# Kernel optimization log

Hardware: AMD Instinct MI355X
Metric: run time of the kernel (lower is better)

The kernel has to match this reference:

```python
import jax, jax.numpy as jnp
import numpy as np

B, L, D, V, T = 4, 512, 2048, 32000, 1024


def setup_inputs() -> dict:
    key = jax.random.key(0)
    k1, k2, k3 = jax.random.split(key, 3)
    encoder_outs = jax.random.normal(k1, (B, L, D), dtype=jnp.float32)
    embed_weight = jax.random.normal(k2, (V, D), dtype=jnp.float32) * 0.02
    input_ids = jax.random.randint(k3, (B, T), 0, V)
    # encoder (audio) tokens occupy the prefix of the LLM input sequence
    modality_mask = jnp.broadcast_to(jnp.arange(T) < L, (B, T))
    return {
        "encoder_outs": encoder_outs,
        "embed_weight": embed_weight,
        "input_ids": input_ids,
        "modality_mask": modality_mask,
    }


def reference(encoder_outs, embed_weight, input_ids, modality_mask):
    # chunked matmul in torch == one big contraction: (B,L,D) x (V,D) -> (B,L,V)
    sim = jnp.einsum("bld,vd->blv", encoder_outs, embed_weight)
    enc_norm = jnp.sqrt(jnp.sum(jnp.square(encoder_outs), axis=-1, keepdims=True))
    w_norm = jnp.sqrt(jnp.sum(jnp.square(embed_weight), axis=-1))  # (V,)
    cosine = sim / enc_norm / w_norm[None, None, :]
    quantize_index = jnp.argmax(cosine, axis=-1)  # (B, L)
    enc_quant = embed_weight[quantize_index]      # (B, L, D) gather lookup

    inputs_embeds = embed_weight[input_ids]       # (B, T, D)
    # pad encoder tokens to full sequence length, then blend via modality mask
    enc_pad = jnp.pad(enc_quant, ((0, 0), (0, T - L), (0, 0)))
    blended = jnp.where(modality_mask[:, :, None], enc_pad, inputs_embeds)
    return blended, quantize_index
```

## Files before the change

kernel.cpp:

```cpp
#include <hip/hip_runtime.h>
#include <hip/hip_fp8.h>
#include <math.h>

typedef __attribute__((ext_vector_type(8))) short short8v;
typedef __attribute__((ext_vector_type(4))) float f32x4;
typedef unsigned long long u64;
typedef unsigned short ushort_t;
typedef unsigned char u8;

constexpr int Bb = 4;
constexpr int Ll = 512;
constexpr int Dk = 2048;
constexpr int Vv = 32000;
constexpr int Tt = 1024;
constexpr int Mrows = Bb * Ll;

constexpr int BM = 256;
constexpr int BN = 256;
constexpr int BK = 64;
constexpr int NKT = Dk / BK;
constexpr int NBX = Mrows / BM;
constexpr int NBY = Vv / BN;
constexpr int NWG = NBX * NBY;
constexpr int CHUNK = NWG / 8;
constexpr int TILE_BYTES = 32 * 512;

constexpr int KCAND = 8;
constexpr int CAND_STRIDE = 500;

constexpr int FBM = 128;
constexpr int FBN = 128;
constexpr int FNVB = Vv / FBN;

constexpr size_t WS_NEEDED = 16842752ull + 65536000ull;

__device__ __forceinline__ unsigned int fkey(float f) {
    unsigned int u = __float_as_uint(f);
    return (u & 0x80000000u) ? ~u : (u | 0x80000000u);
}
__device__ __forceinline__ void top2(u64& b1, u64& b2, u64 p) {
    if (p > b1) { b2 = b1; b1 = p; }
    else if (p > b2) { b2 = p; }
}
__device__ __forceinline__ u64 shfl64(u64 x, int m) {
    unsigned lo = __shfl_xor((unsigned)x, m, 64);
    unsigned hi = __shfl_xor((unsigned)(x >> 32), m, 64);
    return ((u64)hi << 32) | lo;
}
__device__ __forceinline__ u8 to_e4m3(float x) {
    __hip_fp8_e4m3 q(x);
    return q.__x;
}
__device__ __forceinline__ void gload_lds16(const void* g, void* l) {
    __builtin_amdgcn_global_load_lds(
        (const __attribute__((address_space(1))) unsigned int*)g,
        (__attribute__((address_space(3))) unsigned int*)l, 16, 0, 0);
}

__global__ __launch_bounds__(256) void convertA_fp8(const float* __restrict__ A,
                                                    u8* __restrict__ At) {
    const int row = blockIdx.x * 4 + (threadIdx.x >> 6);
    const int lane = threadIdx.x & 63;
    const int bx = row >> 8, rg = (row & 255) >> 4, r15 = row & 15;
    const float* src = A + (size_t)row * Dk;
#pragma unroll
    for (int i = 0; i < 4; ++i) {
        const int k0 = (i * 64 + lane) * 8;
        float4 x = *(const float4*)(src + k0);
        float4 y = *(const float4*)(src + k0 + 4);
        u8 o[8] = {to_e4m3(x.x), to_e4m3(x.y), to_e4m3(x.z), to_e4m3(x.w),
                   to_e4m3(y.x), to_e4m3(y.y), to_e4m3(y.z), to_e4m3(y.w)};
        const int t = k0 >> 6, c = (k0 >> 5) & 1, lp = r15 + ((k0 >> 3) & 3) * 16;
        *(u64*)(At + ((size_t)(bx * NKT + t) * 32 + rg * 2 + c) * 512 + lp * 8) =
            *(const u64*)o;
    }
}

__global__ __launch_bounds__(256) void convertW_fp8(const float* __restrict__ W,
                                                    u8* __restrict__ Wt,
                                                    float* __restrict__ winv) {
    const int row = blockIdx.x * 4 + (threadIdx.x >> 6);
    const int lane = threadIdx.x & 63;
    const int by = row >> 8, rg = (row & 255) >> 4, r15 = row & 15;
    const float* src = W + (size_t)row * Dk;
    float sq = 0.f;
#pragma unroll
    for (int i = 0; i < 4; ++i) {
        const int k0 = (i * 64 + lane) * 8;
        float4 x = *(const float4*)(src + k0);
        float4 y = *(const float4*)(src + k0 + 4);
        sq = fmaf(x.x, x.x, sq); sq = fmaf(x.y, x.y, sq);
        sq = fmaf(x.z, x.z, sq); sq = fmaf(x.w, x.w, sq);
        sq = fmaf(y.x, y.x, sq); sq = fmaf(y.y, y.y, sq);
        sq = fmaf(y.z, y.z, sq); sq = fmaf(y.w, y.w, sq);
        u8 o[8] = {to_e4m3(x.x * 64.f), to_e4m3(x.y * 64.f), to_e4m3(x.z * 64.f),
                   to_e4m3(x.w * 64.f), to_e4m3(y.x * 64.f), to_e4m3(y.y * 64.f),
                   to_e4m3(y.z * 64.f), to_e4m3(y.w * 64.f)};
        const int t = k0 >> 6, c = (k0 >> 5) & 1, lp = r15 + ((k0 >> 3) & 3) * 16;
        *(u64*)(Wt + ((size_t)(by * NKT + t) * 32 + rg * 2 + c) * 512 + lp * 8) =
            *(const u64*)o;
    }
#pragma unroll
    for (int off = 32; off; off >>= 1) sq += __shfl_down(sq, off, 64);
    if (lane == 0) winv[row] = 1.0f / sqrtf(sq);
}

__global__ __launch_bounds__(256) void wnorm_kernel(const float* __restrict__ W,
                                                    float* __restrict__ winv) {
    int wave = (blockIdx.x * blockDim.x + threadIdx.x) >> 6;
    int lane = threadIdx.x & 63;
    if (wave >= Vv) return;
    const float4* row = (const float4*)(W + (size_t)wave * Dk);
    float s = 0.f;
#pragma unroll
    for (int i = 0; i < Dk / 4 / 64; ++i) {
        float4 v = row[lane + 64 * i];
        s = fmaf(v.x, v.x, s); s = fmaf(v.y, v.y, s);
        s = fmaf(v.z, v.z, s); s = fmaf(v.w, v.w, s);
    }
#pragma unroll
    for (int off = 32; off; off >>= 1) s += __shfl_down(s, off, 64);
    if (lane == 0) winv[wave] = 1.0f / sqrtf(s);
}

__global__ void init_best_kernel(u64* __restrict__ best) {
    int i = blockIdx.x * blockDim.x + threadIdx.x;
    if (i < Mrows) best[i] = 0ull;
}

__global__ __launch_bounds__(1024, 4) void score_topk_kernel(
    const u8* __restrict__ At, const u8* __restrict__ Wt,
    const float* __restrict__ winv, u64* __restrict__ cand) {
    __shared__ __align__(16) u8 Alds[2][TILE_BYTES];
    __shared__ __align__(16) u8 Wlds[2][TILE_BYTES];

    const int orig = blockIdx.x;
    const int swz = (orig & 7) * CHUNK + (orig >> 3);
    const int bx = swz & (NBX - 1);
    const int by = swz >> 3;
    const int row0 = bx * BM;
    const int v0 = by * BN;

    const int tid = threadIdx.x;
    const int lane = tid & 63;
    const int w = tid >> 6;
    const int wrr = w >> 2;
    const int wcc = w & 3;

    const u8* sA = At + (size_t)bx * NKT * TILE_BYTES + w * 1024 + lane * 16;
    const u8* sW = Wt + (size_t)by * NKT * TILE_BYTES + w * 1024 + lane * 16;

    f32x4 acc[4][4];
#pragma unroll
    for (int i = 0; i < 4; ++i)
#pragma unroll
        for (int j = 0; j < 4; ++j) acc[i][j] = (f32x4){0.f, 0.f, 0.f, 0.f};

    gload_lds16(sA, &Alds[0][w * 1024]);
    gload_lds16(sW, &Wlds[0][w * 1024]);
    __syncthreads();

    int cur = 0;
    for (int t = 0; t < NKT; ++t) {
        if (t + 1 < NKT) {
            const size_t off = (size_t)(t + 1) * TILE_BYTES;
            gload_lds16(sA + off, &Alds[cur ^ 1][w * 1024]);
            gload_lds16(sW + off, &Wlds[cur ^ 1][w * 1024]);
        }
        __builtin_amdgcn_s_setprio(1);
#pragma unroll
        for (int c = 0; c < 2; ++c) {
            long long a[4], b[4];
#pragma unroll
            for (int m = 0; m < 4; ++m)
                a[m] = *(const long long*)&Alds[cur][(((wrr * 4 + m) * 2 + c) * 64 + lane) * 8];
#pragma unroll
            for (int n = 0; n < 4; ++n)
                b[n] = *(const long long*)&Wlds[cur][(((wcc * 4 + n) * 2 + c) * 64 + lane) * 8];
#pragma unroll
            for (int m = 0; m < 4; ++m)
#pragma unroll
                for (int n = 0; n < 4; ++n)
                    acc[m][n] = __builtin_amdgcn_mfma_f32_16x16x32_fp8_fp8(
                        a[m], b[n], acc[m][n], 0, 0, 0);
        }
        __builtin_amdgcn_s_setprio(0);
        __syncthreads();
        cur ^= 1;
    }

    const int cb = lane & 15;
    float wv[4];
#pragma unroll
    for (int n = 0; n < 4; ++n) wv[n] = winv[v0 + wcc * 64 + n * 16 + cb];

    u64(*red)[8] = (u64(*)[8]) & Alds[0][0];
#pragma unroll
    for (int m = 0; m < 4; ++m) {
#pragma unroll
        for (int reg = 0; reg < 4; ++reg) {
            u64 b1 = 0, b2 = 0;
#pragma unroll
            for (int n = 0; n < 4; ++n) {
                float s = acc[m][n][reg] * wv[n];
                int v = v0 + wcc * 64 + n * 16 + cb;
                u64 p = ((u64)fkey(s) << 32) | (unsigned)(Vv - 1 - v);
                top2(b1, b2, p);
            }
#pragma unroll
            for (int msk = 1; msk < 16; msk <<= 1) {
                u64 o1 = shfl64(b1, msk);
                u64 o2 = shfl64(b2, msk);
                top2(b1, b2, o1);
                top2(b1, b2, o2);
            }
            if (cb == 0) {
                int rl = wrr * 64 + m * 16 + ((lane >> 4) << 2) + reg;
                red[rl][wcc * 2] = b1;
                red[rl][wcc * 2 + 1] = b2;
            }
        }
    }
    __syncthreads();
    if (tid < BM) {
        u64 b1 = red[tid][0], b2 = red[tid][1];
#pragma unroll
        for (int j = 2; j < 8; ++j) top2(b1, b2, red[tid][j]);
        u64* c = cand + (size_t)(row0 + tid) * CAND_STRIDE + by * 2;
        c[0] = b1;
        c[1] = b2;
    }
}

template <typename LdsT>
__device__ __forceinline__ void topk_epilogue_f(f32x4 (&acc)[4][4], LdsT* ldsbase,
                                                const float* __restrict__ winv,
                                                u64* __restrict__ cand, int row0, int v0,
                                                int vby, int tid, int lane, int wr,
                                                int wc) {
    const int cbase = v0 + wc * 64 + (lane & 15);
    float wv[4];
#pragma unroll
    for (int nf = 0; nf < 4; ++nf) wv[nf] = winv[cbase + nf * 16];

    u64(*red)[4] = (u64(*)[4])ldsbase;
#pragma unroll
    for (int mf = 0; mf < 4; ++mf) {
#pragma unroll
        for (int reg = 0; reg < 4; ++reg) {
            u64 b1 = 0, b2 = 0;
#pragma unroll
            for (int nf = 0; nf < 4; ++nf) {
                float s = acc[mf][nf][reg] * wv[nf];
                int v = cbase + nf * 16;
                u64 p = ((u64)fkey(s) << 32) | (unsigned)(Vv - 1 - v);
                top2(b1, b2, p);
            }
#pragma unroll
            for (int m = 1; m < 16; m <<= 1) {
                u64 o1 = shfl64(b1, m);
                u64 o2 = shfl64(b2, m);
                top2(b1, b2, o1);
                top2(b1, b2, o2);
            }
            if ((lane & 15) == 0) {
                int rl = wr * 64 + mf * 16 + ((lane >> 4) << 2) + reg;
                red[rl][wc * 2] = b1;
                red[rl][wc * 2 + 1] = b2;
            }
        }
    }
    __syncthreads();
    if (tid < FBM) {
        u64 b1 = red[tid][0], b2 = red[tid][1];
        top2(b1, b2, red[tid][2]);
        top2(b1, b2, red[tid][3]);
        u64* c = cand + (size_t)(row0 + tid) * CAND_STRIDE + vby * 2;
        c[0] = b1;
        c[1] = b2;
    }
}

__global__ __launch_bounds__(256) void score_topk_fallback(
    const float* __restrict__ A, const float* __restrict__ W,
    const float* __restrict__ winv, u64* __restrict__ cand) {
    __shared__ __align__(16) short Albuf[4096];
    __shared__ __align__(16) short Wlbuf[4096];

    const int tid = threadIdx.x;
    const int row0 = blockIdx.x * FBM;
    const int v0 = blockIdx.y * FBN;
    const int lane = tid & 63;
    const int wid = tid >> 6;
    const int wr = wid >> 1, wc = wid & 1;

    const int rA = ((tid >> 6) << 4) + (tid & 15);
    const int kk = ((tid >> 4) & 3) * 8;

    const float* pa = A + (size_t)(row0 + rA) * Dk + kk;
    const float* pw = W + (size_t)(v0 + rA) * Dk + kk;

    float4 fa0, fa1, fa2, fa3, fw0, fw1, fw2, fw3;
    auto ld4 = [](const float* p) { return *(const float4*)p; };
    auto load_regs = [&](int k0) {
        fa0 = ld4(pa + k0); fa1 = ld4(pa + k0 + 4);
        fa2 = ld4(pa + k0 + (size_t)64 * Dk); fa3 = ld4(pa + k0 + (size_t)64 * Dk + 4);
        fw0 = ld4(pw + k0); fw1 = ld4(pw + k0 + 4);
        fw2 = ld4(pw + k0 + (size_t)64 * Dk); fw3 = ld4(pw + k0 + (size_t)64 * Dk + 4);
    };
    auto pk = [](float lo, float hi) {
        return (int)((__float_as_uint(lo) >> 16) | (__float_as_uint(hi) & 0xFFFF0000u));
    };
    auto cv = [&](float4 a, float4 b) {
        int4 r; r.x = pk(a.x, a.y); r.y = pk(a.z, a.w);
        r.z = pk(b.x, b.y); r.w = pk(b.z, b.w); return r;
    };
    auto write_lds = [&]() {
        *(int4*)(Albuf + tid * 8) = cv(fa0, fa1);
        *(int4*)(Albuf + tid * 8 + 2048) = cv(fa2, fa3);
        *(int4*)(Wlbuf + tid * 8) = cv(fw0, fw1);
        *(int4*)(Wlbuf + tid * 8 + 2048) = cv(fw2, fw3);
    };

    f32x4 acc[4][4];
#pragma unroll
    for (int i = 0; i < 4; ++i)
#pragma unroll
        for (int j = 0; j < 4; ++j) acc[i][j] = (f32x4){0.f, 0.f, 0.f, 0.f};

    load_regs(0);
    for (int kt = 0; kt < Dk / 32; ++kt) {
        write_lds();
        __syncthreads();
        if (kt + 1 < Dk / 32) load_regs((kt + 1) * 32);
        short8v af[4], bf[4];
        const short8v* Ap = (const short8v*)Albuf;
        const short8v* Wp = (const short8v*)Wlbuf;
#pragma unroll
        for (int mf = 0; mf < 4; ++mf) af[mf] = Ap[(wr * 4 + mf) * 64 + lane];
#pragma unroll
        for (int nf = 0; nf < 4; ++nf) bf[nf] = Wp[(wc * 4 + nf) * 64 + lane];
#pragma unroll
        for (int mf = 0; mf < 4; ++mf)
#pragma unroll
            for (int nf = 0; nf < 4; ++nf)
                acc[mf][nf] = __builtin_amdgcn_mfma_f32_16x16x32_bf16(
                    af[mf], bf[nf], acc[mf][nf], 0, 0, 0);
        __syncthreads();
    }

    topk_epilogue_f(acc, Albuf, winv, cand, row0, v0, blockIdx.y, tid, lane, wr, wc);
}

__global__ __launch_bounds__(256) void topk_kernel(const u64* __restrict__ cand,
                                                   int* __restrict__ sel, int nents) {
    int row = blockIdx.x * 4 + (threadIdx.x >> 6);
    int lane = threadIdx.x & 63;
    if (row >= Mrows) return;
    const u64* c = cand + (size_t)row * CAND_STRIDE;
    u64 v[8];
#pragma unroll
    for (int i = 0; i < 8; ++i) {
        int idx = lane + i * 64;
        v[i] = (idx < nents) ? c[idx] : 0ull;
    }
#pragma unroll
    for (int it = 0; it < KCAND; ++it) {
        u64 lm = 0;
#pragma unroll
        for (int i = 0; i < 8; ++i) lm = v[i] > lm ? v[i] : lm;
#pragma unroll
        for (int m = 32; m; m >>= 1) {
            u64 o = shfl64(lm, m);
            lm = o > lm ? o : lm;
        }
#pragma unroll
        for (int i = 0; i < 8; ++i)
            if (v[i] == lm) v[i] = 0;
        if (lane == 0) sel[row * KCAND + it] = Vv - 1 - (int)(unsigned)(lm & 0xFFFFFFFFu);
    }
}

__global__ __launch_bounds__(256) void rescore_kernel(
    const float* __restrict__ A, const float* __restrict__ W,
    const float* __restrict__ winv, const int* __restrict__ sel,
    u64* __restrict__ best) {
    int gw = (int)((blockIdx.x * blockDim.x + threadIdx.x) >> 6);
    int lane = threadIdx.x & 63;
    if (gw >= Mrows * KCAND) return;
    int row = gw >> 3, c = gw & 7;
    int v = sel[row * KCAND + c];
    const float4* a = (const float4*)(A + (size_t)row * Dk);
    const float4* w = (const float4*)(W + (size_t)v * Dk);
    float s = 0.f;
#pragma unroll
    for (int i = 0; i < Dk / 4 / 64; ++i) {
        float4 x = a[lane + 64 * i], y = w[lane + 64 * i];
        s = fmaf(x.x, y.x, s); s = fmaf(x.y, y.y, s);
        s = fmaf(x.z, y.z, s); s = fmaf(x.w, y.w, s);
    }
#pragma unroll
    for (int m = 32; m; m >>= 1) s += __shfl_xor(s, m, 64);
    if (lane == 0) {
        u64 p = ((u64)fkey(s * winv[v]) << 32) | (unsigned)(Vv - 1 - v);
        atomicMax(best + row, p);
    }
}

__global__ __launch_bounds__(256) void blend_kernel(
    const float* __restrict__ emb, const int* __restrict__ ids,
    const u64* __restrict__ best, float* __restrict__ out) {
    int row = blockIdx.x;
    int b = row / Tt;
    int t = row % Tt;
    int idx;
    if (t < Ll) {
        idx = Vv - 1 - (int)(best[b * Ll + t] & 0xFFFFFFFFu);
    } else {
        idx = ids[row];
    }
    const float4* src = (const float4*)(emb + (size_t)idx * Dk);
    float4* dst = (float4*)(out + (size_t)row * Dk);
    for (int i = threadIdx.x; i < Dk / 4; i += blockDim.x) dst[i] = src[i];
    if (t < Ll && threadIdx.x == 0) {
        out[(size_t)Bb * Tt * Dk + (size_t)(b * Ll + t)] = (float)idx;
    }
}

extern "C" void kernel_launch(void* const* d_in, const int* in_sizes, int n_in,
                              void* d_out, int out_size, void* d_ws, size_t ws_size,
                              hipStream_t stream) {
    const float* encoder_outs = (const float*)d_in[0];
    const float* embed_weight = (const float*)d_in[1];
    const int* input_ids = (const int*)d_in[2];

    float* out = (float*)d_out;

    float* winv = (float*)d_ws;
    u64* best = (u64*)((char*)d_ws + 131072);
    int* sel = (int*)((char*)d_ws + 147456);
    u64* cand = (u64*)((char*)d_ws + 262144);
    u8* At = (u8*)((char*)d_ws + 8454144);
    u8* Wt = (u8*)((char*)d_ws + 16842752);

    init_best_kernel<<<(Mrows + 255) / 256, 256, 0, stream>>>(best);

    if (ws_size >= WS_NEEDED) {
        convertA_fp8<<<Mrows / 4, 256, 0, stream>>>(encoder_outs, At);
        convertW_fp8<<<Vv / 4, 256, 0, stream>>>(embed_weight, Wt, winv);
        score_topk_kernel<<<NWG, 1024, 0, stream>>>(At, Wt, winv, cand);
        topk_kernel<<<Mrows / 4, 256, 0, stream>>>(cand, sel, 2 * NBY);
    } else {
        wnorm_kernel<<<Vv * 64 / 256, 256, 0, stream>>>(embed_weight, winv);
        dim3 grid(Mrows / FBM, Vv / FBN);
        score_topk_fallback<<<grid, 256, 0, stream>>>(encoder_outs, embed_weight, winv,
                                                      cand);
        topk_kernel<<<Mrows / 4, 256, 0, stream>>>(cand, sel, 2 * FNVB);
    }
    rescore_kernel<<<Mrows * KCAND / 4, 256, 0, stream>>>(encoder_outs, embed_weight,
                                                          winv, sel, best);
    blend_kernel<<<Bb * Tt, 256, 0, stream>>>(embed_weight, input_ids, best, out);
}
```

Measured before the change: 947.6 us.

## Load FP8 GEMM fragments directly from global into registers, dropping LDS staging

The fp8 scoring GEMM no longer stages A and W tiles through double-buffered LDS with global_load_lds and per-step barriers. Each wave now loads 16-byte fragments straight from global memory into registers, with two register buffers in flight. The conversion kernels rewrite the packed layout so that one 16-byte load covers both k-halves. The workgroup shrinks to 512 threads, each wave computing 8x4 MFMA tiles. This removes LDS traffic and __syncthreads, but operands shared across waves are now re-read from global/L2 instead of reused from LDS, and register pressure rises.

Result: slower. 1.346 ms (+42.0%).

```diff
diff --git a/kernel.cpp b/kernel.cpp
--- a/kernel.cpp
+++ b/kernel.cpp
@@ -4,6 +4,7 @@
 
 typedef __attribute__((ext_vector_type(8))) short short8v;
 typedef __attribute__((ext_vector_type(4))) float f32x4;
+typedef __attribute__((ext_vector_type(2))) long long i64x2;
 typedef unsigned long long u64;
 typedef unsigned short ushort_t;
 typedef unsigned char u8;
@@ -17,13 +18,12 @@
 
 constexpr int BM = 256;
 constexpr int BN = 256;
-constexpr int BK = 64;
-constexpr int NKT = Dk / BK;
+constexpr int NKT = 32;
 constexpr int NBX = Mrows / BM;
 constexpr int NBY = Vv / BN;
 constexpr int NWG = NBX * NBY;
 constexpr int CHUNK = NWG / 8;
-constexpr int TILE_BYTES = 32 * 512;
+constexpr int TSTRIDE = 16 * 1024;
 
 constexpr int KCAND = 8;
 constexpr int CAND_STRIDE = 500;
@@ -50,11 +50,6 @@
 __device__ __forceinline__ u8 to_e4m3(float x) {
     __hip_fp8_e4m3 q(x);
     return q.__x;
-}
-__device__ __forceinline__ void gload_lds16(const void* g, void* l) {
-    __builtin_amdgcn_global_load_lds(
-        (const __attribute__((address_space(1))) unsigned int*)g,
-        (__attribute__((address_space(3))) unsigned int*)l, 16, 0, 0);
 }
 
 __global__ __launch_bounds__(256) void convertA_fp8(const float* __restrict__ A,
@@ -71,7 +66,7 @@
         u8 o[8] = {to_e4m3(x.x), to_e4m3(x.y), to_e4m3(x.z), to_e4m3(x.w),
                    to_e4m3(y.x), to_e4m3(y.y), to_e4m3(y.z), to_e4m3(y.w)};
         const int t = k0 >> 6, c = (k0 >> 5) & 1, lp = r15 + ((k0 >> 3) & 3) * 16;
-        *(u64*)(At + ((size_t)(bx * NKT + t) * 32 + rg * 2 + c) * 512 + lp * 8) =
+        *(u64*)(At + ((size_t)(bx * NKT + t) * 16 + rg) * 1024 + lp * 16 + c * 8) =
             *(const u64*)o;
     }
 }
@@ -97,7 +92,7 @@
                    to_e4m3(x.w * 64.f), to_e4m3(y.x * 64.f), to_e4m3(y.y * 64.f),
                    to_e4m3(y.z * 64.f), to_e4m3(y.w * 64.f)};
         const int t = k0 >> 6, c = (k0 >> 5) & 1, lp = r15 + ((k0 >> 3) & 3) * 16;
-        *(u64*)(Wt + ((size_t)(by * NKT + t) * 32 + rg * 2 + c) * 512 + lp * 8) =
+        *(u64*)(Wt + ((size_t)(by * NKT + t) * 16 + rg) * 1024 + lp * 16 + c * 8) =
             *(const u64*)o;
     }
 #pragma unroll
@@ -128,11 +123,10 @@
     if (i < Mrows) best[i] = 0ull;
 }
 
-__global__ __launch_bounds__(1024, 4) void score_topk_kernel(
+__global__ __launch_bounds__(512, 2) void score_topk_kernel(
     const u8* __restrict__ At, const u8* __restrict__ Wt,
     const float* __restrict__ winv, u64* __restrict__ cand) {
-    __shared__ __align__(16) u8 Alds[2][TILE_BYTES];
-    __shared__ __align__(16) u8 Wlds[2][TILE_BYTES];
+    __shared__ __align__(16) u64 red[256][8];
 
     const int orig = blockIdx.x;
     const int swz = (orig & 7) * CHUNK + (orig >> 3);
@@ -144,66 +138,61 @@
     const int tid = threadIdx.x;
     const int lane = tid & 63;
     const int w = tid >> 6;
-    const int wrr = w >> 2;
-    const int wcc = w & 3;
-
-    const u8* sA = At + (size_t)bx * NKT * TILE_BYTES + w * 1024 + lane * 16;
-    const u8* sW = Wt + (size_t)by * NKT * TILE_BYTES + w * 1024 + lane * 16;
-
-    f32x4 acc[4][4];
-#pragma unroll
-    for (int i = 0; i < 4; ++i)
+    const int wr = w >> 2;
+    const int wc = w & 3;
+
+    const u8* pA = At + (size_t)bx * NKT * TSTRIDE + (wr * 8) * 1024 + lane * 16;
+    const u8* pW = Wt + (size_t)by * NKT * TSTRIDE + (wc * 4) * 1024 + lane * 16;
+
+    f32x4 acc[8][4];
+#pragma unroll
+    for (int i = 0; i < 8; ++i)
 #pragma unroll
         for (int j = 0; j < 4; ++j) acc[i][j] = (f32x4){0.f, 0.f, 0.f, 0.f};
 
-    gload_lds16(sA, &Alds[0][w * 1024]);
-    gload_lds16(sW, &Wlds[0][w * 1024]);
-    __syncthreads();
-
-    int cur = 0;
-    for (int t = 0; t < NKT; ++t) {
-        if (t + 1 < NKT) {
-            const size_t off = (size_t)(t + 1) * TILE_BYTES;
-            gload_lds16(sA + off, &Alds[cur ^ 1][w * 1024]);
-            gload_lds16(sW + off, &Wlds[cur ^ 1][w * 1024]);
-        }
-        __builtin_amdgcn_s_setprio(1);
-#pragma unroll
-        for (int c = 0; c < 2; ++c) {
-            long long a[4], b[4];
-#pragma unroll
-            for (int m = 0; m < 4; ++m)
-                a[m] = *(const long long*)&Alds[cur][(((wrr * 4 + m) * 2 + c) * 64 + lane) * 8];
-#pragma unroll
-            for (int n = 0; n < 4; ++n)
-                b[n] = *(const long long*)&Wlds[cur][(((wcc * 4 + n) * 2 + c) * 64 + lane) * 8];
-#pragma unroll
-            for (int m = 0; m < 4; ++m)
+    i64x2 fa0[8], fw0[4], fa1[8], fw1[4];
+    auto LD = [&](int t, i64x2 (&fa)[8], i64x2 (&fw)[4]) {
+        const u8* qa = pA + (size_t)t * TSTRIDE;
+        const u8* qw = pW + (size_t)t * TSTRIDE;
+#pragma unroll
+        for (int m = 0; m < 8; ++m) fa[m] = *(const i64x2*)(qa + m * 1024);
+#pragma unroll
+        for (int n = 0; n < 4; ++n) fw[n] = *(const i64x2*)(qw + n * 1024);
+    };
+    auto MM = [&](i64x2 (&fa)[8], i64x2 (&fw)[4]) {
+#pragma unroll
+        for (int c = 0; c < 2; ++c)
+#pragma unroll
+            for (int m = 0; m < 8; ++m)
 #pragma unroll
                 for (int n = 0; n < 4; ++n)
                     acc[m][n] = __builtin_amdgcn_mfma_f32_16x16x32_fp8_fp8(
-                        a[m], b[n], acc[m][n], 0, 0, 0);
-        }
-        __builtin_amdgcn_s_setprio(0);
-        __syncthreads();
-        cur ^= 1;
+                        fa[m][c], fw[n][c], acc[m][n], 0, 0, 0);
+    };
+
+    LD(0, fa0, fw0);
+    LD(1, fa1, fw1);
+    for (int t = 0; t < NKT; t += 2) {
+        MM(fa0, fw0);
+        if (t + 2 < NKT) LD(t + 2, fa0, fw0);
+        MM(fa1, fw1);
+        if (t + 3 < NKT) LD(t + 3, fa1, fw1);
     }
 
     const int cb = lane & 15;
     float wv[4];
 #pragma unroll
-    for (int n = 0; n < 4; ++n) wv[n] = winv[v0 + wcc * 64 + n * 16 + cb];
-
-    u64(*red)[8] = (u64(*)[8]) & Alds[0][0];
-#pragma unroll
-    for (int m = 0; m < 4; ++m) {
+    for (int n = 0; n < 4; ++n) wv[n] = winv[v0 + wc * 64 + n * 16 + cb];
+
+#pragma unroll
+    for (int m = 0; m < 8; ++m) {
 #pragma unroll
         for (int reg = 0; reg < 4; ++reg) {
             u64 b1 = 0, b2 = 0;
 #pragma unroll
             for (int n = 0; n < 4; ++n) {
                 float s = acc[m][n][reg] * wv[n];
-                int v = v0 + wcc * 64 + n * 16 + cb;
+                int v = v0 + wc * 64 + n * 16 + cb;
                 u64 p = ((u64)fkey(s) << 32) | (unsigned)(Vv - 1 - v);
                 top2(b1, b2, p);
             }
@@ -215,9 +204,9 @@
                 top2(b1, b2, o2);
             }
             if (cb == 0) {
-                int rl = wrr * 64 + m * 16 + ((lane >> 4) << 2) + reg;
-                red[rl][wcc * 2] = b1;
-                red[rl][wcc * 2 + 1] = b2;
+                int rl = wr * 128 + m * 16 + ((lane >> 4) << 2) + reg;
+                red[rl][wc * 2] = b1;
+                red[rl][wc * 2 + 1] = b2;
             }
         }
     }
@@ -448,7 +437,7 @@
     if (ws_size >= WS_NEEDED) {
         convertA_fp8<<<Mrows / 4, 256, 0, stream>>>(encoder_outs, At);
         convertW_fp8<<<Vv / 4, 256, 0, stream>>>(embed_weight, Wt, winv);
-        score_topk_kernel<<<NWG, 1024, 0, stream>>>(At, Wt, winv, cand);
+        score_topk_kernel<<<NWG, 512, 0, stream>>>(At, Wt, winv, cand);
         topk_kernel<<<Mrows / 4, 256, 0, stream>>>(cand, sel, 2 * NBY);
     } else {
         wnorm_kernel<<<Vv * 64 / 256, 256, 0, stream>>>(embed_weight, winv);
```
